# Performance work log

Hardware: AMD Instinct MI355X
Metric: run time of the kernel (lower is better)

Reference implementation:

```python
import jax, jax.numpy as jnp
import numpy as np

NEG_SLOPE = 0.01  # torch nn.LeakyReLU default


def setup_inputs() -> dict:
    key = jax.random.key(0)
    k1, k2 = jax.random.split(key)
    B, L, N = 32, 512, 1024
    X = jax.random.normal(k1, (B, L, N), dtype=jnp.float32)
    W = jax.random.normal(k2, (1, 2 * L), dtype=jnp.float32) * (1.0 / np.sqrt(2 * L))
    return {"X": X, "W": W}


def reference(X, W):
    # X: [B, L, N]; W: [1, 2L] weight of Linear(2L, 1, bias=False)
    L = X.shape[1]
    N = X.shape[2]
    w1 = W[0, :L]   # applied to X[:, :, i]
    w2 = W[0, L:]   # applied to X[:, :, j]
    s1 = jnp.einsum('bln,l->bn', X, w1)  # [B, N]
    s2 = jnp.einsum('bln,l->bn', X, w2)  # [B, N]
    # e[b,i,j] = leaky_relu(s1[b,i] + s2[b,j]) for i != j, 0 on the diagonal
    e = jax.nn.leaky_relu(s1[:, :, None] + s2[:, None, :], NEG_SLOPE)  # [B, N, N]
    diag = jnp.eye(N, dtype=bool)
    e = jnp.where(diag[None, :, :], 0.0, e)
    # softmax over dim=1 (over i), matching torch.softmax(e, dim=1)
    alpha = jax.nn.softmax(e, axis=1)  # [B, N, N]
    # h = bmm(alpha, X^T)^T: h[b,l,i] = sum_j alpha[b,i,j] * X[b,l,j]
    h = jnp.einsum('bij,blj->bli', alpha, X)  # [B, L, N]
    return jax.nn.sigmoid(h)
```

## Files before the change

kernel.cpp:

```cpp
#include <hip/hip_runtime.h>
#include <hip/hip_bf16.h>

#define BATCH 32
#define LSEQ  512
#define NDIM  1024
#define NSPLIT 16

typedef __attribute__((ext_vector_type(8))) short bf16x8;
typedef __attribute__((ext_vector_type(4))) float f32x4;

__device__ __forceinline__ unsigned short f2bf(float x) {
    __hip_bfloat16 h = __float2bfloat16(x);
    return __builtin_bit_cast(unsigned short, h);
}

__global__ __launch_bounds__(256) void prep_kernel(
    const float* __restrict__ X, const float* __restrict__ W,
    unsigned short* __restrict__ Xb, float* __restrict__ P1, float* __restrict__ P2)
{
    __shared__ float sw[2 * LSEQ];
    int tid = threadIdx.x;
    for (int i = tid; i < 2 * LSEQ; i += 256) sw[i] = W[i];
    __syncthreads();

    int b  = blockIdx.y;
    int sp = blockIdx.x;
    int l0 = sp * (LSEQ / NSPLIT);
    size_t base = ((size_t)b * LSEQ + l0) * NDIM + tid * 4;
    const float* xp = X + base;
    unsigned short* xbp = Xb + base;

    float a0=0,a1=0,a2=0,a3=0, c0=0,c1=0,c2=0,c3=0;
    for (int l = 0; l < LSEQ / NSPLIT; ++l) {
        float4 x = *(const float4*)(xp + (size_t)l * NDIM);
        float w1 = sw[l0 + l], w2 = sw[LSEQ + l0 + l];
        a0 = fmaf(x.x, w1, a0); a1 = fmaf(x.y, w1, a1);
        a2 = fmaf(x.z, w1, a2); a3 = fmaf(x.w, w1, a3);
        c0 = fmaf(x.x, w2, c0); c1 = fmaf(x.y, w2, c1);
        c2 = fmaf(x.z, w2, c2); c3 = fmaf(x.w, w2, c3);
        ushort4 u; u.x = f2bf(x.x); u.y = f2bf(x.y); u.z = f2bf(x.z); u.w = f2bf(x.w);
        *(ushort4*)(xbp + (size_t)l * NDIM) = u;
    }
    size_t po = ((size_t)sp * BATCH + b) * NDIM + tid * 4;
    *(float4*)(P1 + po) = make_float4(a0, a1, a2, a3);
    *(float4*)(P2 + po) = make_float4(c0, c1, c2, c3);
}

__global__ __launch_bounds__(256) void stats_kernel(
    const float* __restrict__ P1, const float* __restrict__ P2,
    float* __restrict__ s1, float* __restrict__ s2, float* __restrict__ rd)
{
    __shared__ float s1s[NDIM];
    __shared__ float s2s[128];
    int t = threadIdx.x;
    int b = blockIdx.x >> 3, sl = blockIdx.x & 7;
    int j0 = sl * 128;

    #pragma unroll
    for (int q = 0; q < 4; ++q) {
        int n = q * 256 + t;
        float a = 0.f;
        #pragma unroll
        for (int sp = 0; sp < NSPLIT; ++sp)
            a += P1[((size_t)sp * BATCH + b) * NDIM + n];
        s1s[n] = a;
        if (sl == 0) s1[b * NDIM + n] = a;
    }
    if (t < 128) {
        int j = j0 + t;
        float c = 0.f;
        #pragma unroll
        for (int sp = 0; sp < NSPLIT; ++sp)
            c += P2[((size_t)sp * BATCH + b) * NDIM + j];
        s2s[t] = c;
        s2[b * NDIM + j] = c;
    }
    __syncthreads();

    int jl = t >> 1, half = t & 1;
    int jg = j0 + jl;
    float s2j = s2s[jl];
    float sum = 0.f;
    int i0 = half * 512;
    for (int i = i0; i < i0 + 512; ++i) {
        float v = s1s[i] + s2j;
        v = fmaxf(v, 0.01f * v);
        if (i == jg) v = 0.f;
        sum += __expf(v);
    }
    sum += __shfl_xor(sum, 1);
    if (half == 0) rd[b * NDIM + jg] = 1.0f / sum;
}

__global__ __launch_bounds__(256) void gemm_kernel(
    const unsigned short* __restrict__ Xb,
    const float* __restrict__ s1, const float* __restrict__ s2,
    const float* __restrict__ rd, float* __restrict__ out)
{
    __shared__ __align__(16) unsigned short Xs[128 * 32];
    __shared__ __align__(16) unsigned short Bs[128 * 32];

    int tid = threadIdx.x, wid = tid >> 6, lane = tid & 63;
    int wm = wid >> 1, wn = wid & 1;

    int flat = blockIdx.x;
    int xcd   = flat & 7;
    int idx   = flat >> 3;
    int bg    = idx >> 5;
    int inner = idx & 31;
    int b  = bg * 8 + xcd;
    int n0 = (inner & 7) * 128;
    int l0 = (inner >> 3) * 128;

    const unsigned short* Xg = Xb + ((size_t)b * LSEQ + l0) * NDIM;
    const float* s2b = s2 + b * NDIM;
    const float* rdb = rd + b * NDIM;

    int rin = lane >> 2, ch = lane & 3;

    int an   = tid >> 1;
    int koff = (tid & 1) * 16;
    float s1i = s1[b * NDIM + n0 + an];

    f32x4 acc[4][4] = {};

    for (int kb = 0; kb < 32; ++kb) {
        int k0 = kb * 32;
        __syncthreads();

        #pragma unroll
        for (int q = 0; q < 2; ++q) {
            int row = wid * 32 + q * 16 + rin;
            const unsigned short* gx = Xg + (size_t)row * NDIM + k0 + ch * 8;
            unsigned short* lx = &Xs[(wid * 32 + q * 16) * 32];
            __builtin_amdgcn_global_load_lds(
                (const __attribute__((address_space(1))) void*)gx,
                (__attribute__((address_space(3))) void*)lx, 16, 0, 0);
        }

        {
            int kg0 = k0 + koff;
            float sv[16], rv[16];
            #pragma unroll
            for (int q = 0; q < 4; ++q) {
                float4 s4 = *(const float4*)(s2b + kg0 + q * 4);
                float4 r4 = *(const float4*)(rdb + kg0 + q * 4);
                sv[q*4+0]=s4.x; sv[q*4+1]=s4.y; sv[q*4+2]=s4.z; sv[q*4+3]=s4.w;
                rv[q*4+0]=r4.x; rv[q*4+1]=r4.y; rv[q*4+2]=r4.z; rv[q*4+3]=r4.w;
            }
            bf16x8 v0, v1;
            #pragma unroll
            for (int k = 0; k < 16; ++k) {
                float v = s1i + sv[k];
                v = fmaxf(v, 0.01f * v);
                if (n0 + an == kg0 + k) v = 0.f;
                float a = __expf(v) * rv[k];
                unsigned short u = f2bf(a);
                if (k < 8) v0[k] = (short)u; else v1[k - 8] = (short)u;
            }
            *(bf16x8*)&Bs[an * 32 + koff]     = v0;
            *(bf16x8*)&Bs[an * 32 + koff + 8] = v1;
        }
        __syncthreads();

        bf16x8 av[4], bv[4];
        int rsel = lane & 15, ksel = (lane >> 4) * 8;
        #pragma unroll
        for (int mi = 0; mi < 4; ++mi)
            av[mi] = *(const bf16x8*)&Xs[(wm * 64 + mi * 16 + rsel) * 32 + ksel];
        #pragma unroll
        for (int ni = 0; ni < 4; ++ni)
            bv[ni] = *(const bf16x8*)&Bs[(wn * 64 + ni * 16 + rsel) * 32 + ksel];
        #pragma unroll
        for (int mi = 0; mi < 4; ++mi)
            #pragma unroll
            for (int ni = 0; ni < 4; ++ni)
                acc[mi][ni] = __builtin_amdgcn_mfma_f32_16x16x32_bf16(
                    av[mi], bv[ni], acc[mi][ni], 0, 0, 0);
    }

    float* outb = out + ((size_t)b * LSEQ + l0) * NDIM + n0;
    int rq = lane >> 4, cl = lane & 15;
    #pragma unroll
    for (int mi = 0; mi < 4; ++mi)
        #pragma unroll
        for (int ni = 0; ni < 4; ++ni) {
            int col = wn * 64 + ni * 16 + cl;
            #pragma unroll
            for (int r2 = 0; r2 < 4; ++r2) {
                int row = wm * 64 + mi * 16 + rq * 4 + r2;
                float v = acc[mi][ni][r2];
                outb[(size_t)row * NDIM + col] = 1.0f / (1.0f + __expf(-v));
            }
        }
}

extern "C" void kernel_launch(void* const* d_in, const int* in_sizes, int n_in,
                              void* d_out, int out_size, void* d_ws, size_t ws_size,
                              hipStream_t stream) {
    (void)in_sizes; (void)n_in; (void)out_size; (void)ws_size;
    const float* X = (const float*)d_in[0];
    const float* W = (const float*)d_in[1];
    float* out = (float*)d_out;

    float* s1 = (float*)d_ws;
    float* s2 = s1 + BATCH * NDIM;
    float* rd = s2 + BATCH * NDIM;
    float* P1 = rd + BATCH * NDIM;
    float* P2 = P1 + (size_t)NSPLIT * BATCH * NDIM;
    unsigned short* Xb = (unsigned short*)(P2 + (size_t)NSPLIT * BATCH * NDIM);

    prep_kernel<<<dim3(NSPLIT, BATCH), 256, 0, stream>>>(X, W, Xb, P1, P2);
    stats_kernel<<<256, 256, 0, stream>>>(P1, P2, s1, s2, rd);
    gemm_kernel<<<1024, 256, 0, stream>>>(Xb, s1, s2, rd, out);
}
```

Measured before the change: 212.4 us.

## Materialize attention matrix in separate kernel and stream it into GEMM

Moves computation of the bf16 softmax attention matrix out of the GEMM inner loop into a new btgen kernel that writes a full B×N×N bf16 buffer. The GEMM then loads both operands from global memory via direct-to-LDS loads and processes 64-wide K steps per barrier pair. This removes the redundant exp recomputation done by each of the four L-tiles sharing a batch/column tile. In exchange it adds about 64MB of write and repeated read traffic plus an extra launch.

```diff
diff --git a/kernel.cpp b/kernel.cpp
--- a/kernel.cpp
+++ b/kernel.cpp
@@ -92,13 +92,47 @@
     if (half == 0) rd[b * NDIM + jg] = 1.0f / sum;
 }
 
+__global__ __launch_bounds__(256) void btgen_kernel(
+    const float* __restrict__ s1, const float* __restrict__ s2,
+    const float* __restrict__ rd, unsigned short* __restrict__ Bt)
+{
+    int wid = threadIdx.x >> 6, lane = threadIdx.x & 63;
+    int r = blockIdx.x * 4 + wid;
+    int b = r >> 10, i = r & 1023;
+    float s1i = s1[r];
+    const float* s2b = s2 + b * NDIM;
+    const float* rdb = rd + b * NDIM;
+    unsigned short* outp = Bt + (size_t)r * NDIM;
+
+    #pragma unroll
+    for (int q = 0; q < 2; ++q) {
+        int j0 = q * 512 + lane * 8;
+        float sv[8], rv[8];
+        #pragma unroll
+        for (int h = 0; h < 2; ++h) {
+            float4 s4 = *(const float4*)(s2b + j0 + h * 4);
+            float4 r4 = *(const float4*)(rdb + j0 + h * 4);
+            sv[h*4+0]=s4.x; sv[h*4+1]=s4.y; sv[h*4+2]=s4.z; sv[h*4+3]=s4.w;
+            rv[h*4+0]=r4.x; rv[h*4+1]=r4.y; rv[h*4+2]=r4.z; rv[h*4+3]=r4.w;
+        }
+        bf16x8 v;
+        #pragma unroll
+        for (int k = 0; k < 8; ++k) {
+            float e = s1i + sv[k];
+            e = fmaxf(e, 0.01f * e);
+            if (j0 + k == i) e = 0.f;
+            v[k] = (short)f2bf(__expf(e) * rv[k]);
+        }
+        *(bf16x8*)&outp[j0] = v;
+    }
+}
+
 __global__ __launch_bounds__(256) void gemm_kernel(
-    const unsigned short* __restrict__ Xb,
-    const float* __restrict__ s1, const float* __restrict__ s2,
-    const float* __restrict__ rd, float* __restrict__ out)
-{
-    __shared__ __align__(16) unsigned short Xs[128 * 32];
-    __shared__ __align__(16) unsigned short Bs[128 * 32];
+    const unsigned short* __restrict__ Xb, const unsigned short* __restrict__ Bt,
+    float* __restrict__ out)
+{
+    __shared__ __align__(16) unsigned short Xs[2 * 128 * 32];
+    __shared__ __align__(16) unsigned short Bs[2 * 128 * 32];
 
     int tid = threadIdx.x, wid = tid >> 6, lane = tid & 63;
     int wm = wid >> 1, wn = wid & 1;
@@ -113,70 +147,52 @@
     int l0 = (inner >> 3) * 128;
 
     const unsigned short* Xg = Xb + ((size_t)b * LSEQ + l0) * NDIM;
-    const float* s2b = s2 + b * NDIM;
-    const float* rdb = rd + b * NDIM;
+    const unsigned short* Bg = Bt + ((size_t)b * NDIM + n0) * NDIM;
 
     int rin = lane >> 2, ch = lane & 3;
 
-    int an   = tid >> 1;
-    int koff = (tid & 1) * 16;
-    float s1i = s1[b * NDIM + n0 + an];
-
     f32x4 acc[4][4] = {};
 
-    for (int kb = 0; kb < 32; ++kb) {
-        int k0 = kb * 32;
+    for (int kb = 0; kb < 16; ++kb) {
+        int k0 = kb * 64;
         __syncthreads();
-
-        #pragma unroll
-        for (int q = 0; q < 2; ++q) {
-            int row = wid * 32 + q * 16 + rin;
-            const unsigned short* gx = Xg + (size_t)row * NDIM + k0 + ch * 8;
-            unsigned short* lx = &Xs[(wid * 32 + q * 16) * 32];
-            __builtin_amdgcn_global_load_lds(
-                (const __attribute__((address_space(1))) void*)gx,
-                (__attribute__((address_space(3))) void*)lx, 16, 0, 0);
-        }
-
-        {
-            int kg0 = k0 + koff;
-            float sv[16], rv[16];
-            #pragma unroll
-            for (int q = 0; q < 4; ++q) {
-                float4 s4 = *(const float4*)(s2b + kg0 + q * 4);
-                float4 r4 = *(const float4*)(rdb + kg0 + q * 4);
-                sv[q*4+0]=s4.x; sv[q*4+1]=s4.y; sv[q*4+2]=s4.z; sv[q*4+3]=s4.w;
-                rv[q*4+0]=r4.x; rv[q*4+1]=r4.y; rv[q*4+2]=r4.z; rv[q*4+3]=r4.w;
+        #pragma unroll
+        for (int kh = 0; kh < 2; ++kh) {
+            #pragma unroll
+            for (int q = 0; q < 2; ++q) {
+                int row = wid * 32 + q * 16 + rin;
+                int kg = k0 + kh * 32 + ch * 8;
+                const unsigned short* gx = Xg + (size_t)row * NDIM + kg;
+                const unsigned short* gb = Bg + (size_t)row * NDIM + kg;
+                unsigned short* lx = &Xs[kh * 4096 + (wid * 32 + q * 16) * 32];
+                unsigned short* lb = &Bs[kh * 4096 + (wid * 32 + q * 16) * 32];
+                __builtin_amdgcn_global_load_lds(
+                    (const __attribute__((address_space(1))) void*)gx,
+                    (__attribute__((address_space(3))) void*)lx, 16, 0, 0);
+                __builtin_amdgcn_global_load_lds(
+                    (const __attribute__((address_space(1))) void*)gb,
+                    (__attribute__((address_space(3))) void*)lb, 16, 0, 0);
             }
-            bf16x8 v0, v1;
-            #pragma unroll
-            for (int k = 0; k < 16; ++k) {
-                float v = s1i + sv[k];
-                v = fmaxf(v, 0.01f * v);
-                if (n0 + an == kg0 + k) v = 0.f;
-                float a = __expf(v) * rv[k];
-                unsigned short u = f2bf(a);
-                if (k < 8) v0[k] = (short)u; else v1[k - 8] = (short)u;
-            }
-            *(bf16x8*)&Bs[an * 32 + koff]     = v0;
-            *(bf16x8*)&Bs[an * 32 + koff + 8] = v1;
         }
         __syncthreads();
 
-        bf16x8 av[4], bv[4];
         int rsel = lane & 15, ksel = (lane >> 4) * 8;
         #pragma unroll
-        for (int mi = 0; mi < 4; ++mi)
-            av[mi] = *(const bf16x8*)&Xs[(wm * 64 + mi * 16 + rsel) * 32 + ksel];
-        #pragma unroll
-        for (int ni = 0; ni < 4; ++ni)
-            bv[ni] = *(const bf16x8*)&Bs[(wn * 64 + ni * 16 + rsel) * 32 + ksel];
-        #pragma unroll
-        for (int mi = 0; mi < 4; ++mi)
+        for (int kh = 0; kh < 2; ++kh) {
+            bf16x8 av[4], bv[4];
+            #pragma unroll
+            for (int mi = 0; mi < 4; ++mi)
+                av[mi] = *(const bf16x8*)&Xs[kh * 4096 + (wm * 64 + mi * 16 + rsel) * 32 + ksel];
             #pragma unroll
             for (int ni = 0; ni < 4; ++ni)
-                acc[mi][ni] = __builtin_amdgcn_mfma_f32_16x16x32_bf16(
-                    av[mi], bv[ni], acc[mi][ni], 0, 0, 0);
+                bv[ni] = *(const bf16x8*)&Bs[kh * 4096 + (wn * 64 + ni * 16 + rsel) * 32 + ksel];
+            #pragma unroll
+            for (int mi = 0; mi < 4; ++mi)
+                #pragma unroll
+                for (int ni = 0; ni < 4; ++ni)
+                    acc[mi][ni] = __builtin_amdgcn_mfma_f32_16x16x32_bf16(
+                        av[mi], bv[ni], acc[mi][ni], 0, 0, 0);
+        }
     }
 
     float* outb = out + ((size_t)b * LSEQ + l0) * NDIM + n0;
@@ -209,8 +225,10 @@
     float* P1 = rd + BATCH * NDIM;
     float* P2 = P1 + (size_t)NSPLIT * BATCH * NDIM;
     unsigned short* Xb = (unsigned short*)(P2 + (size_t)NSPLIT * BATCH * NDIM);
+    unsigned short* Bt = Xb + (size_t)BATCH * LSEQ * NDIM;
 
     prep_kernel<<<dim3(NSPLIT, BATCH), 256, 0, stream>>>(X, W, Xb, P1, P2);
     stats_kernel<<<256, 256, 0, stream>>>(P1, P2, s1, s2, rd);
-    gemm_kernel<<<1024, 256, 0, stream>>>(Xb, s1, s2, rd, out);
-}
+    btgen_kernel<<<(BATCH * NDIM) / 4, 256, 0, stream>>>(s1, s2, rd, Bt);
+    gemm_kernel<<<1024, 256, 0, stream>>>(Xb, Bt, out);
+}
```

New measurement: 198.2 us. 6.7% less time.

## Materialize bf16 attention matrix in stats kernel and double-buffer GEMM loads

Applied to the files above, without the earlier changes.

The stats kernel now writes the full normalized attention matrix Bt (B×N×N in bf16) to workspace, so the GEMM no longer recomputes exp/leaky-relu for its B tile on every k-step. The GEMM then loads both operands with global_load_lds into double-buffered LDS, prefetching the next k-slice while MFMAs run on the current one, synchronized by explicit vmcnt waits and barriers. This trades per-block recomputation for an extra write and read of a large bf16 matrix in global memory, and relies on hand-written waitcnt correctness.

```diff
diff --git a/kernel.cpp b/kernel.cpp
--- a/kernel.cpp
+++ b/kernel.cpp
@@ -12,6 +12,12 @@
 __device__ __forceinline__ unsigned short f2bf(float x) {
     __hip_bfloat16 h = __float2bfloat16(x);
     return __builtin_bit_cast(unsigned short, h);
+}
+
+__device__ __forceinline__ void glds16(const unsigned short* g, unsigned short* l) {
+    __builtin_amdgcn_global_load_lds(
+        (const __attribute__((address_space(1))) void*)g,
+        (__attribute__((address_space(3))) void*)l, 16, 0, 0);
 }
 
 __global__ __launch_bounds__(256) void prep_kernel(
@@ -46,12 +52,13 @@
     *(float4*)(P2 + po) = make_float4(c0, c1, c2, c3);
 }
 
-__global__ __launch_bounds__(256) void stats_kernel(
+__global__ __launch_bounds__(256) void statsbt_kernel(
     const float* __restrict__ P1, const float* __restrict__ P2,
-    float* __restrict__ s1, float* __restrict__ s2, float* __restrict__ rd)
+    unsigned short* __restrict__ Bt)
 {
     __shared__ float s1s[NDIM];
     __shared__ float s2s[128];
+    __shared__ float rds[128];
     int t = threadIdx.x;
     int b = blockIdx.x >> 3, sl = blockIdx.x & 7;
     int j0 = sl * 128;
@@ -64,7 +71,6 @@
         for (int sp = 0; sp < NSPLIT; ++sp)
             a += P1[((size_t)sp * BATCH + b) * NDIM + n];
         s1s[n] = a;
-        if (sl == 0) s1[b * NDIM + n] = a;
     }
     if (t < 128) {
         int j = j0 + t;
@@ -73,32 +79,56 @@
         for (int sp = 0; sp < NSPLIT; ++sp)
             c += P2[((size_t)sp * BATCH + b) * NDIM + j];
         s2s[t] = c;
-        s2[b * NDIM + j] = c;
     }
     __syncthreads();
 
-    int jl = t >> 1, half = t & 1;
-    int jg = j0 + jl;
-    float s2j = s2s[jl];
-    float sum = 0.f;
-    int i0 = half * 512;
-    for (int i = i0; i < i0 + 512; ++i) {
-        float v = s1s[i] + s2j;
-        v = fmaxf(v, 0.01f * v);
-        if (i == jg) v = 0.f;
-        sum += __expf(v);
-    }
-    sum += __shfl_xor(sum, 1);
-    if (half == 0) rd[b * NDIM + jg] = 1.0f / sum;
+    {
+        int jl = t >> 1, half = t & 1;
+        int jg = j0 + jl;
+        float s2j = s2s[jl];
+        float sum = 0.f;
+        int i0 = half * 512;
+        for (int i = i0; i < i0 + 512; ++i) {
+            float v = s1s[i] + s2j;
+            v = fmaxf(v, 0.01f * v);
+            if (i == jg) v = 0.f;
+            sum += __expf(v);
+        }
+        sum += __shfl_xor(sum, 1);
+        if (half == 0) rds[jl] = 1.0f / sum;
+    }
+    __syncthreads();
+
+    int jq = (t & 31) * 4;
+    int ir = t >> 5;
+    float4 s2v = *(const float4*)&s2s[jq];
+    float4 rdv = *(const float4*)&rds[jq];
+    unsigned short* outp = Bt + (size_t)b * NDIM * NDIM + j0 + jq;
+    for (int i = ir; i < NDIM; i += 8) {
+        float s1i = s1s[i];
+        float e0 = s1i + s2v.x, e1 = s1i + s2v.y, e2 = s1i + s2v.z, e3 = s1i + s2v.w;
+        e0 = fmaxf(e0, 0.01f*e0); e1 = fmaxf(e1, 0.01f*e1);
+        e2 = fmaxf(e2, 0.01f*e2); e3 = fmaxf(e3, 0.01f*e3);
+        int jg = j0 + jq;
+        if (jg + 0 == i) e0 = 0.f;
+        if (jg + 1 == i) e1 = 0.f;
+        if (jg + 2 == i) e2 = 0.f;
+        if (jg + 3 == i) e3 = 0.f;
+        ushort4 u;
+        u.x = f2bf(__expf(e0) * rdv.x);
+        u.y = f2bf(__expf(e1) * rdv.y);
+        u.z = f2bf(__expf(e2) * rdv.z);
+        u.w = f2bf(__expf(e3) * rdv.w);
+        *(ushort4*)(outp + (size_t)i * NDIM) = u;
+    }
 }
 
 __global__ __launch_bounds__(256) void gemm_kernel(
-    const unsigned short* __restrict__ Xb,
-    const float* __restrict__ s1, const float* __restrict__ s2,
-    const float* __restrict__ rd, float* __restrict__ out)
+    const unsigned short* __restrict__ Xb, const unsigned short* __restrict__ Bt,
+    float* __restrict__ out)
 {
-    __shared__ __align__(16) unsigned short Xs[128 * 32];
-    __shared__ __align__(16) unsigned short Bs[128 * 32];
+    __shared__ __align__(16) unsigned short Xs[2][128 * 32];
+    __shared__ __align__(16) unsigned short Bs[2][128 * 32];
 
     int tid = threadIdx.x, wid = tid >> 6, lane = tid & 63;
     int wm = wid >> 1, wn = wid & 1;
@@ -113,70 +143,46 @@
     int l0 = (inner >> 3) * 128;
 
     const unsigned short* Xg = Xb + ((size_t)b * LSEQ + l0) * NDIM;
-    const float* s2b = s2 + b * NDIM;
-    const float* rdb = rd + b * NDIM;
+    const unsigned short* Bg = Bt + ((size_t)b * NDIM + n0) * NDIM;
 
     int rin = lane >> 2, ch = lane & 3;
-
-    int an   = tid >> 1;
-    int koff = (tid & 1) * 16;
-    float s1i = s1[b * NDIM + n0 + an];
+    int srow0 = wid * 32, srow1 = wid * 32 + 16;
+
+    glds16(Xg + (size_t)(srow0 + rin) * NDIM + ch * 8, &Xs[0][srow0 * 32]);
+    glds16(Bg + (size_t)(srow0 + rin) * NDIM + ch * 8, &Bs[0][srow0 * 32]);
+    glds16(Xg + (size_t)(srow1 + rin) * NDIM + ch * 8, &Xs[0][srow1 * 32]);
+    glds16(Bg + (size_t)(srow1 + rin) * NDIM + ch * 8, &Bs[0][srow1 * 32]);
 
     f32x4 acc[4][4] = {};
+    int rsel = lane & 15, ksel = (lane >> 4) * 8;
 
     for (int kb = 0; kb < 32; ++kb) {
-        int k0 = kb * 32;
-        __syncthreads();
-
-        #pragma unroll
-        for (int q = 0; q < 2; ++q) {
-            int row = wid * 32 + q * 16 + rin;
-            const unsigned short* gx = Xg + (size_t)row * NDIM + k0 + ch * 8;
-            unsigned short* lx = &Xs[(wid * 32 + q * 16) * 32];
-            __builtin_amdgcn_global_load_lds(
-                (const __attribute__((address_space(1))) void*)gx,
-                (__attribute__((address_space(3))) void*)lx, 16, 0, 0);
-        }
-
-        {
-            int kg0 = k0 + koff;
-            float sv[16], rv[16];
-            #pragma unroll
-            for (int q = 0; q < 4; ++q) {
-                float4 s4 = *(const float4*)(s2b + kg0 + q * 4);
-                float4 r4 = *(const float4*)(rdb + kg0 + q * 4);
-                sv[q*4+0]=s4.x; sv[q*4+1]=s4.y; sv[q*4+2]=s4.z; sv[q*4+3]=s4.w;
-                rv[q*4+0]=r4.x; rv[q*4+1]=r4.y; rv[q*4+2]=r4.z; rv[q*4+3]=r4.w;
-            }
-            bf16x8 v0, v1;
-            #pragma unroll
-            for (int k = 0; k < 16; ++k) {
-                float v = s1i + sv[k];
-                v = fmaxf(v, 0.01f * v);
-                if (n0 + an == kg0 + k) v = 0.f;
-                float a = __expf(v) * rv[k];
-                unsigned short u = f2bf(a);
-                if (k < 8) v0[k] = (short)u; else v1[k - 8] = (short)u;
-            }
-            *(bf16x8*)&Bs[an * 32 + koff]     = v0;
-            *(bf16x8*)&Bs[an * 32 + koff + 8] = v1;
-        }
-        __syncthreads();
+        int cur = kb & 1;
+        int nxt = cur ^ 1;
+        int knext = ((kb + 1) & 31) * 32;
+
+        glds16(Xg + (size_t)(srow0 + rin) * NDIM + knext + ch * 8, &Xs[nxt][srow0 * 32]);
+        glds16(Bg + (size_t)(srow0 + rin) * NDIM + knext + ch * 8, &Bs[nxt][srow0 * 32]);
+        glds16(Xg + (size_t)(srow1 + rin) * NDIM + knext + ch * 8, &Xs[nxt][srow1 * 32]);
+        glds16(Bg + (size_t)(srow1 + rin) * NDIM + knext + ch * 8, &Bs[nxt][srow1 * 32]);
+
+        asm volatile("s_waitcnt vmcnt(4)\n\ts_barrier" ::: "memory");
 
         bf16x8 av[4], bv[4];
-        int rsel = lane & 15, ksel = (lane >> 4) * 8;
         #pragma unroll
         for (int mi = 0; mi < 4; ++mi)
-            av[mi] = *(const bf16x8*)&Xs[(wm * 64 + mi * 16 + rsel) * 32 + ksel];
+            av[mi] = *(const bf16x8*)&Xs[cur][(wm * 64 + mi * 16 + rsel) * 32 + ksel];
         #pragma unroll
         for (int ni = 0; ni < 4; ++ni)
-            bv[ni] = *(const bf16x8*)&Bs[(wn * 64 + ni * 16 + rsel) * 32 + ksel];
+            bv[ni] = *(const bf16x8*)&Bs[cur][(wn * 64 + ni * 16 + rsel) * 32 + ksel];
         #pragma unroll
         for (int mi = 0; mi < 4; ++mi)
             #pragma unroll
             for (int ni = 0; ni < 4; ++ni)
                 acc[mi][ni] = __builtin_amdgcn_mfma_f32_16x16x32_bf16(
                     av[mi], bv[ni], acc[mi][ni], 0, 0, 0);
+
+        asm volatile("s_barrier" ::: "memory");
     }
 
     float* outb = out + ((size_t)b * LSEQ + l0) * NDIM + n0;
@@ -203,14 +209,12 @@
     const float* W = (const float*)d_in[1];
     float* out = (float*)d_out;
 
-    float* s1 = (float*)d_ws;
-    float* s2 = s1 + BATCH * NDIM;
-    float* rd = s2 + BATCH * NDIM;
-    float* P1 = rd + BATCH * NDIM;
+    float* P1 = (float*)d_ws;
     float* P2 = P1 + (size_t)NSPLIT * BATCH * NDIM;
     unsigned short* Xb = (unsigned short*)(P2 + (size_t)NSPLIT * BATCH * NDIM);
+    unsigned short* Bt = Xb + (size_t)BATCH * LSEQ * NDIM;
 
     prep_kernel<<<dim3(NSPLIT, BATCH), 256, 0, stream>>>(X, W, Xb, P1, P2);
-    stats_kernel<<<256, 256, 0, stream>>>(P1, P2, s1, s2, rd);
-    gemm_kernel<<<1024, 256, 0, stream>>>(Xb, s1, s2, rd, out);
-}
+    statsbt_kernel<<<256, 256, 0, stream>>>(P1, P2, Bt);
+    gemm_kernel<<<1024, 256, 0, stream>>>(Xb, Bt, out);
+}
```

After: 211.1 us. About the same (-0.6%).
